# Kernel optimization log

Hardware: AMD Instinct MI355X
Metric: run time of the kernel (lower is better)

## Reference

```python
import jax, jax.numpy as jnp
import numpy as np

N_NODES = 50000
N_EDGES = 800000
F_IN = 128
HIDDEN = 256
N_CLASSES = 4


def setup_inputs() -> dict:
    key = jax.random.key(0)
    k1, k2, k3, k4 = jax.random.split(key, 4)
    x = jax.random.normal(k1, (N_NODES, F_IN), dtype=jnp.float32)
    edge_index = jax.random.randint(k2, (2, N_EDGES), 0, N_NODES, dtype=jnp.int64)
    # Glorot-style init for the two GCNConv linear layers (PyG GCNConv: W then bias)
    s1 = (6.0 / (F_IN + HIDDEN)) ** 0.5
    s2 = (6.0 / (HIDDEN + N_CLASSES)) ** 0.5
    W1 = jax.random.uniform(k3, (F_IN, HIDDEN), jnp.float32, -s1, s1)
    W2 = jax.random.uniform(k4, (HIDDEN, N_CLASSES), jnp.float32, -s2, s2)
    b1 = jnp.zeros((HIDDEN,), jnp.float32)
    b2 = jnp.zeros((N_CLASSES,), jnp.float32)
    return {"x": x, "edge_index": edge_index, "W1": W1, "b1": b1, "W2": W2, "b2": b2}


def _gcn_conv(x, W, b, src, dst, n_nodes):
    # PyG GCNConv: h = x @ W; add self-loops; symmetric D^{-1/2}(A+I)D^{-1/2} aggregation; + bias
    h = x @ W                                            # [N, out]
    deg = jnp.zeros((n_nodes,), h.dtype).at[dst].add(1.0) + 1.0  # +1 for self-loop
    dis = jax.lax.rsqrt(deg)                             # deg^{-1/2}
    norm = dis[src] * dis[dst]                           # [E]
    msg = norm[:, None] * h[src]                         # [E, out] per-edge messages
    agg = jax.ops.segment_sum(msg, dst, num_segments=n_nodes)
    agg = agg + (dis * dis)[:, None] * h                 # self-loop contribution
    return agg + b


def reference(x, edge_index, W1, b1, W2, b2):
    src, dst = edge_index[0], edge_index[1]
    h = _gcn_conv(x, W1, b1, src, dst, N_NODES)
    h = jax.nn.relu(h)
    # F.dropout with training=False (eval/inference reference) is identity
    out = _gcn_conv(h, W2, b2, src, dst, N_NODES)
    return out
```

## Files before the change

### kernel.cpp

```cpp
#include <hip/hip_runtime.h>

#define F_IN   128
#define HIDDEN 256
#define NCLS   4

#define BSH    7
#define BNODES 128
#define BCAP   3072
#define CHUNK  4096

typedef __attribute__((ext_vector_type(8))) short short8;
typedef __attribute__((ext_vector_type(4))) float f32x4;

__device__ __forceinline__ unsigned short f2bf(float f) {
    unsigned int u = __float_as_uint(f);
    return (unsigned short)((u + 0x7fffu + ((u >> 16) & 1u)) >> 16);
}

__device__ __forceinline__ float bflo(unsigned int u) { return __uint_as_float(u << 16); }
__device__ __forceinline__ float bfhi(unsigned int u) { return __uint_as_float(u & 0xffff0000u); }


__global__ __launch_bounds__(256) void k_bin(const int* __restrict__ srcIdx,
                                             const int* __restrict__ dstIdx,
                                             int* __restrict__ cursor,
                                             unsigned int* __restrict__ inter,
                                             int E, int nbuk) {
    __shared__ int cntS[512], bA[512], bB[512], curS[512], eS[512], gS[512];
    __shared__ unsigned int stag[CHUNK];
    __shared__ unsigned short bb[CHUNK];
    int t = threadIdx.x;
    int e0 = blockIdx.x * CHUNK;
    int n = E - e0; if (n > CHUNK) n = CHUNK;

    cntS[t] = 0; cntS[t + 256] = 0;
    __syncthreads();
    for (int i = t; i < n; i += 256)
        atomicAdd(&cntS[dstIdx[e0 + i] >> BSH], 1);
    __syncthreads();

    int* pa = bA; int* pb = bB;
    bA[t] = cntS[t]; bA[t + 256] = cntS[t + 256];
    __syncthreads();
    for (int off = 1; off < 512; off <<= 1) {
        pb[t] = pa[t] + (t >= off ? pa[t - off] : 0);
        int p1 = t + 256;
        pb[p1] = pa[p1] + (p1 >= off ? pa[p1 - off] : 0);
        __syncthreads();
        int* tmp = pa; pa = pb; pb = tmp;
    }
    eS[t] = pa[t] - cntS[t];
    curS[t] = eS[t];
    int p1 = t + 256;
    eS[p1] = pa[p1] - cntS[p1];
    curS[p1] = eS[p1];
    __syncthreads();

    for (int i = t; i < nbuk; i += 256) {
        int c = cntS[i];
        gS[i] = (c > 0) ? atomicAdd(&cursor[i], c) : 0;
    }
    __syncthreads();

    for (int i = t; i < n; i += 256) {
        int d = dstIdx[e0 + i];
        int s = srcIdx[e0 + i];
        int b = d >> BSH;
        unsigned int w = ((unsigned int)(d & (BNODES - 1)) << 16) | (unsigned int)s;
        int off = atomicAdd(&curS[b], 1);
        stag[off] = w;
        bb[off] = (unsigned short)b;
    }
    __syncthreads();

    for (int i = t; i < n; i += 256) {
        int b = bb[i];
        inter[(size_t)b * BCAP + gS[b] + (i - eS[b])] = stag[i];
    }
}


__global__ __launch_bounds__(512) void k_scan_buckets(const int* __restrict__ cursor,
                                                      int* __restrict__ base, int nbuk) {
    __shared__ int A[512], B[512];
    int t = threadIdx.x;
    int v = (t < nbuk) ? cursor[t] : 0;
    int* pa = A; int* pb = B;
    A[t] = v;
    __syncthreads();
    for (int off = 1; off < 512; off <<= 1) {
        pb[t] = pa[t] + (t >= off ? pa[t - off] : 0);
        __syncthreads();
        int* tmp = pa; pa = pb; pb = tmp;
    }
    if (t < nbuk) base[t] = pa[t] - v;
}


__global__ __launch_bounds__(256) void k_bucket_build(const unsigned int* __restrict__ inter,
                                                      const int* __restrict__ cursor,
                                                      const int* __restrict__ base,
                                                      const float2* __restrict__ x2,
                                                      int* __restrict__ rowptr,
                                                      float* __restrict__ dis,
                                                      unsigned int* __restrict__ xs,
                                                      unsigned short* __restrict__ csr16,
                                                      int N, int E, int nbuk) {
    __shared__ int cntS[BNODES], A[BNODES], B[BNODES], curS[BNODES];
    __shared__ float disS[BNODES];
    int t = threadIdx.x;
    int b = blockIdx.x;
    int node0 = b << BSH;
    int nloc = N - node0; if (nloc > BNODES) nloc = BNODES;
    int cntb = cursor[b];
    int gB = base[b];
    const unsigned int* ip = inter + (size_t)b * BCAP;

    if (t < BNODES) cntS[t] = 0;
    __syncthreads();
    for (int i = t; i < cntb; i += 256)
        atomicAdd(&cntS[ip[i] >> 16], 1);
    __syncthreads();

    int* pa = A; int* pb = B;
    if (t < BNODES) A[t] = cntS[t];
    __syncthreads();
    for (int off = 1; off < BNODES; off <<= 1) {
        if (t < BNODES) pb[t] = pa[t] + (t >= off ? pa[t - off] : 0);
        __syncthreads();
        int* tmp = pa; pa = pb; pb = tmp;
    }
    if (t < BNODES) {
        int excl = pa[t] - cntS[t];
        curS[t] = excl;
        int node = node0 + t;
        if (node < N) {
            rowptr[node] = gB + excl;
            float d = rsqrtf((float)cntS[t] + 1.0f);
            dis[node] = d;
            disS[t] = d;
        }
    }
    if (b == 0 && t == 0) rowptr[N] = E;
    __syncthreads();

    for (int i = t; i < cntb; i += 256) {
        unsigned int w = ip[i];
        int off = atomicAdd(&curS[w >> 16], 1);
        csr16[gB + off] = (unsigned short)(w & 0xffffu);
    }

    for (int i = t; i < nloc * 64; i += 256) {
        int nl = i >> 6, l = i & 63;
        float d = disS[nl];
        float2 v = x2[((size_t)(node0 + nl)) * 64 + l];
        xs[((size_t)(node0 + nl)) * 64 + l] =
            (unsigned int)f2bf(d * v.x) | ((unsigned int)f2bf(d * v.y) << 16);
    }
}


__global__ __launch_bounds__(256) void k_w1f(const float* __restrict__ W1,
                                             unsigned short* __restrict__ W1f) {
    int t = blockIdx.x * 256 + threadIdx.x;
    int lane = t & 63;
    int ks = (t >> 6) & 3;
    int ct = t >> 8;
    int n = ct * 16 + (lane & 15);
    int k0 = ks * 32 + (lane >> 4) * 8;
    unsigned int w[4];
#pragma unroll
    for (int p = 0; p < 4; ++p) {
        unsigned int lo = f2bf(W1[(k0 + 2 * p + 0) * HIDDEN + n]);
        unsigned int hi = f2bf(W1[(k0 + 2 * p + 1) * HIDDEN + n]);
        w[p] = lo | (hi << 16);
    }
    *(uint4*)(W1f + (size_t)t * 8) = make_uint4(w[0], w[1], w[2], w[3]);
}


__global__ __launch_bounds__(256) void k_pull_x(const int* __restrict__ rowptr,
                                                const unsigned short* __restrict__ csr16,
                                                const float* __restrict__ dis,
                                                const unsigned int* __restrict__ xs,
                                                const float2* __restrict__ x2,
                                                unsigned int* __restrict__ aggB, int N) {
    int wave = threadIdx.x >> 6;
    int node = blockIdx.x * 4 + wave;
    int l = threadIdx.x & 63;
    if (node >= N) return;
    int beg = rowptr[node];
    int end = rowptr[node + 1];
    float ax = 0.f, ay = 0.f;
    int e = beg;
    for (; e + 7 < end; e += 8) {
        int s0 = csr16[e + 0], s1 = csr16[e + 1], s2 = csr16[e + 2], s3 = csr16[e + 3];
        int s4 = csr16[e + 4], s5 = csr16[e + 5], s6 = csr16[e + 6], s7 = csr16[e + 7];
        unsigned int u0 = xs[(size_t)s0 * 64 + l];
        unsigned int u1 = xs[(size_t)s1 * 64 + l];
        unsigned int u2 = xs[(size_t)s2 * 64 + l];
        unsigned int u3 = xs[(size_t)s3 * 64 + l];
        unsigned int u4 = xs[(size_t)s4 * 64 + l];
        unsigned int u5 = xs[(size_t)s5 * 64 + l];
        unsigned int u6 = xs[(size_t)s6 * 64 + l];
        unsigned int u7 = xs[(size_t)s7 * 64 + l];
        ax += bflo(u0) + bflo(u1) + bflo(u2) + bflo(u3) + bflo(u4) + bflo(u5) + bflo(u6) + bflo(u7);
        ay += bfhi(u0) + bfhi(u1) + bfhi(u2) + bfhi(u3) + bfhi(u4) + bfhi(u5) + bfhi(u6) + bfhi(u7);
    }
    for (; e < end; ++e) {
        unsigned int u = xs[(size_t)csr16[e] * 64 + l];
        ax += bflo(u);
        ay += bfhi(u);
    }
    float dd = dis[node];
    float sd = dd * dd;
    float2 xv = x2[(size_t)node * 64 + l];
    float ox = dd * ax + sd * xv.x;
    float oy = dd * ay + sd * xv.y;
    aggB[(size_t)node * 64 + l] = (unsigned int)f2bf(ox) | ((unsigned int)f2bf(oy) << 16);
}


__global__ __launch_bounds__(256) void k_gemm_mfma(const unsigned short* __restrict__ aggB,
                                                   const unsigned short* __restrict__ W1f,
                                                   const float* __restrict__ b1,
                                                   const float* __restrict__ W2,
                                                   float* __restrict__ Z, int N) {
    int wave = threadIdx.x >> 6;
    int lane = threadIdx.x & 63;
    int tile = blockIdx.x * 4 + wave;
    int row0 = tile * 16;
    if (row0 >= N) return;
    int q = lane >> 4;
    int c16 = lane & 15;

    short8 a[4];
    const unsigned short* arow = aggB + (size_t)(row0 + c16) * F_IN;
#pragma unroll
    for (int ks = 0; ks < 4; ++ks)
        a[ks] = *(const short8*)(arow + ks * 32 + q * 8);

    float p[4][4] = {{0.f}};
#pragma unroll
    for (int ct = 0; ct < 16; ++ct) {
        f32x4 c = {0.f, 0.f, 0.f, 0.f};
#pragma unroll
        for (int ks = 0; ks < 4; ++ks) {
            short8 b = *(const short8*)(W1f + ((size_t)((ct * 4 + ks) * 64 + lane)) * 8);
            c = __builtin_amdgcn_mfma_f32_16x16x32_bf16(a[ks], b, c, 0, 0, 0);
        }
        int n = ct * 16 + c16;
        float bias = b1[n];
        float4 w2v = *(const float4*)(W2 + n * NCLS);
#pragma unroll
        for (int r = 0; r < 4; ++r) {
            float h = c[r] + bias;
            h = h > 0.f ? h : 0.f;
            p[r][0] += h * w2v.x;
            p[r][1] += h * w2v.y;
            p[r][2] += h * w2v.z;
            p[r][3] += h * w2v.w;
        }
    }
#pragma unroll
    for (int m = 1; m < 16; m <<= 1) {
#pragma unroll
        for (int r = 0; r < 4; ++r) {
#pragma unroll
            for (int j = 0; j < 4; ++j)
                p[r][j] += __shfl_xor(p[r][j], m);
        }
    }
    if (c16 == 0) {
#pragma unroll
        for (int r = 0; r < 4; ++r) {
            int row = row0 + q * 4 + r;
            *(float4*)(Z + (size_t)row * NCLS) = make_float4(p[r][0], p[r][1], p[r][2], p[r][3]);
        }
    }
}


__global__ __launch_bounds__(256) void k_pull_z(const int* __restrict__ rowptr,
                                                const unsigned short* __restrict__ csr16,
                                                const float* __restrict__ dis,
                                                const float* __restrict__ Z,
                                                const float* __restrict__ b2,
                                                float* __restrict__ out, int N) {
    int t = blockIdx.x * blockDim.x + threadIdx.x;
    int node = t >> 2;
    int j = t & 3;
    if (node >= N) return;
    int beg = rowptr[node];
    int end = rowptr[node + 1];
    float acc = 0.f;
    for (int e = beg; e < end; ++e) {
        int s = csr16[e];
        acc += dis[s] * Z[(size_t)s * NCLS + j];
    }
    float dd = dis[node];
    out[(size_t)node * NCLS + j] = dd * acc + dd * dd * Z[(size_t)node * NCLS + j] + b2[j];
}


extern "C" void kernel_launch(void* const* d_in, const int* in_sizes, int n_in,
                              void* d_out, int out_size, void* d_ws, size_t ws_size,
                              hipStream_t stream) {
    const float* x      = (const float*)d_in[0];
    const int*   ei     = (const int*)d_in[1];
    const float* W1     = (const float*)d_in[2];
    const float* b1     = (const float*)d_in[3];
    const float* W2     = (const float*)d_in[4];
    const float* b2     = (const float*)d_in[5];
    float* out          = (float*)d_out;

    const int N = in_sizes[0] / F_IN;
    const int E = in_sizes[1] / 2;
    const int* srcIdx = ei;
    const int* dstIdx = ei + E;

    const int nbuk = (N + BNODES - 1) >> BSH;

    unsigned short* aggB = (unsigned short*)d_ws;
    unsigned short* xsB  = aggB + (size_t)N * F_IN;
    unsigned short* W1f  = xsB + (size_t)N * F_IN;
    float* Z    = (float*)(W1f + 32768);
    float* dis  = Z + (size_t)N * NCLS;
    int* rowptr = (int*)(dis + N);
    int* cursor = rowptr + N + 1;
    int* bucketBase = cursor + nbuk;
    unsigned short* csr16 = (unsigned short*)(bucketBase + nbuk);
    unsigned int* inter = (unsigned int*)(csr16 + ((E + 1) & ~1));

    hipMemsetAsync(cursor, 0, (size_t)nbuk * sizeof(int), stream);
    k_bin<<<(E + CHUNK - 1) / CHUNK, 256, 0, stream>>>(srcIdx, dstIdx, cursor, inter, E, nbuk);
    k_scan_buckets<<<1, 512, 0, stream>>>(cursor, bucketBase, nbuk);
    k_bucket_build<<<nbuk, 256, 0, stream>>>(inter, cursor, bucketBase, (const float2*)x,
                                             rowptr, dis, (unsigned int*)xsB, csr16, N, E, nbuk);

    k_w1f<<<16, 256, 0, stream>>>(W1, W1f);
    k_pull_x<<<(N + 3) / 4, 256, 0, stream>>>(rowptr, csr16, dis, (const unsigned int*)xsB,
                                              (const float2*)x, (unsigned int*)aggB, N);

    const int nTiles = (N + 15) / 16;
    k_gemm_mfma<<<(nTiles + 3) / 4, 256, 0, stream>>>(aggB, W1f, b1, W2, Z, N);

    k_pull_z<<<(N * 4 + 255) / 256, 256, 0, stream>>>(rowptr, csr16, dis, Z, b2, out, N);
}
```

Measured before the change: 183.3 us.

## Fuse neighbor aggregation with MFMA GEMM and fold scan and memset into kernels

Merges the layer-1 gather aggregation and the bf16 MFMA GEMM into one kernel that stages 32 aggregated rows in LDS, then splits the 16 hidden column tiles across 4 waves and reduces the partial layer-2 projections through shared memory. This removes the aggB round trip through global memory and one launch. The bucket prefix scan is recomputed inside each bucket_build block by summing the preceding cursors, and the cursor memset is folded into the W1 conversion kernel, which drops two more launches. The cost is less parallelism per block during the gather phase, since each wave now handles 8 nodes in sequence, and redundant per-block scan reads.

```diff
diff --git a/kernel.cpp b/kernel.cpp
--- a/kernel.cpp
+++ b/kernel.cpp
@@ -8,6 +8,7 @@
 #define BNODES 128
 #define BCAP   3072
 #define CHUNK  4096
+#define MROWS  32
 
 typedef __attribute__((ext_vector_type(8))) short short8;
 typedef __attribute__((ext_vector_type(4))) float f32x4;
@@ -80,41 +81,33 @@
 }
 
 
-__global__ __launch_bounds__(512) void k_scan_buckets(const int* __restrict__ cursor,
-                                                      int* __restrict__ base, int nbuk) {
-    __shared__ int A[512], B[512];
-    int t = threadIdx.x;
-    int v = (t < nbuk) ? cursor[t] : 0;
-    int* pa = A; int* pb = B;
-    A[t] = v;
-    __syncthreads();
-    for (int off = 1; off < 512; off <<= 1) {
-        pb[t] = pa[t] + (t >= off ? pa[t - off] : 0);
-        __syncthreads();
-        int* tmp = pa; pa = pb; pb = tmp;
-    }
-    if (t < nbuk) base[t] = pa[t] - v;
-}
-
-
 __global__ __launch_bounds__(256) void k_bucket_build(const unsigned int* __restrict__ inter,
                                                       const int* __restrict__ cursor,
-                                                      const int* __restrict__ base,
                                                       const float2* __restrict__ x2,
                                                       int* __restrict__ rowptr,
                                                       float* __restrict__ dis,
                                                       unsigned int* __restrict__ xs,
                                                       unsigned short* __restrict__ csr16,
                                                       int N, int E, int nbuk) {
-    __shared__ int cntS[BNODES], A[BNODES], B[BNODES], curS[BNODES];
+    __shared__ int cntS[BNODES], A[BNODES], B[BNODES], curS[BNODES], red[256];
     __shared__ float disS[BNODES];
     int t = threadIdx.x;
     int b = blockIdx.x;
     int node0 = b << BSH;
     int nloc = N - node0; if (nloc > BNODES) nloc = BNODES;
     int cntb = cursor[b];
-    int gB = base[b];
     const unsigned int* ip = inter + (size_t)b * BCAP;
+
+    int partial = 0;
+    for (int i = t; i < b; i += 256) partial += cursor[i];
+    red[t] = partial;
+    __syncthreads();
+    for (int off = 128; off > 0; off >>= 1) {
+        if (t < off) red[t] += red[t + off];
+        __syncthreads();
+    }
+    int gB = red[0];
+    __syncthreads();
 
     if (t < BNODES) cntS[t] = 0;
     __syncthreads();
@@ -160,9 +153,11 @@
 }
 
 
-__global__ __launch_bounds__(256) void k_w1f(const float* __restrict__ W1,
-                                             unsigned short* __restrict__ W1f) {
+__global__ __launch_bounds__(256) void k_w1f_zero(const float* __restrict__ W1,
+                                                  unsigned short* __restrict__ W1f,
+                                                  int* __restrict__ cursor, int nbuk) {
     int t = blockIdx.x * 256 + threadIdx.x;
+    if (t < nbuk) cursor[t] = 0;
     int lane = t & 63;
     int ks = (t >> 6) & 3;
     int ct = t >> 8;
@@ -179,87 +174,89 @@
 }
 
 
-__global__ __launch_bounds__(256) void k_pull_x(const int* __restrict__ rowptr,
-                                                const unsigned short* __restrict__ csr16,
-                                                const float* __restrict__ dis,
-                                                const unsigned int* __restrict__ xs,
-                                                const float2* __restrict__ x2,
-                                                unsigned int* __restrict__ aggB, int N) {
-    int wave = threadIdx.x >> 6;
-    int node = blockIdx.x * 4 + wave;
-    int l = threadIdx.x & 63;
-    if (node >= N) return;
-    int beg = rowptr[node];
-    int end = rowptr[node + 1];
-    float ax = 0.f, ay = 0.f;
-    int e = beg;
-    for (; e + 7 < end; e += 8) {
-        int s0 = csr16[e + 0], s1 = csr16[e + 1], s2 = csr16[e + 2], s3 = csr16[e + 3];
-        int s4 = csr16[e + 4], s5 = csr16[e + 5], s6 = csr16[e + 6], s7 = csr16[e + 7];
-        unsigned int u0 = xs[(size_t)s0 * 64 + l];
-        unsigned int u1 = xs[(size_t)s1 * 64 + l];
-        unsigned int u2 = xs[(size_t)s2 * 64 + l];
-        unsigned int u3 = xs[(size_t)s3 * 64 + l];
-        unsigned int u4 = xs[(size_t)s4 * 64 + l];
-        unsigned int u5 = xs[(size_t)s5 * 64 + l];
-        unsigned int u6 = xs[(size_t)s6 * 64 + l];
-        unsigned int u7 = xs[(size_t)s7 * 64 + l];
-        ax += bflo(u0) + bflo(u1) + bflo(u2) + bflo(u3) + bflo(u4) + bflo(u5) + bflo(u6) + bflo(u7);
-        ay += bfhi(u0) + bfhi(u1) + bfhi(u2) + bfhi(u3) + bfhi(u4) + bfhi(u5) + bfhi(u6) + bfhi(u7);
-    }
-    for (; e < end; ++e) {
-        unsigned int u = xs[(size_t)csr16[e] * 64 + l];
-        ax += bflo(u);
-        ay += bfhi(u);
-    }
-    float dd = dis[node];
-    float sd = dd * dd;
-    float2 xv = x2[(size_t)node * 64 + l];
-    float ox = dd * ax + sd * xv.x;
-    float oy = dd * ay + sd * xv.y;
-    aggB[(size_t)node * 64 + l] = (unsigned int)f2bf(ox) | ((unsigned int)f2bf(oy) << 16);
-}
-
-
-__global__ __launch_bounds__(256) void k_gemm_mfma(const unsigned short* __restrict__ aggB,
-                                                   const unsigned short* __restrict__ W1f,
-                                                   const float* __restrict__ b1,
-                                                   const float* __restrict__ W2,
-                                                   float* __restrict__ Z, int N) {
-    int wave = threadIdx.x >> 6;
-    int lane = threadIdx.x & 63;
-    int tile = blockIdx.x * 4 + wave;
-    int row0 = tile * 16;
-    if (row0 >= N) return;
-    int q = lane >> 4;
-    int c16 = lane & 15;
-
-    short8 a[4];
-    const unsigned short* arow = aggB + (size_t)(row0 + c16) * F_IN;
-#pragma unroll
-    for (int ks = 0; ks < 4; ++ks)
-        a[ks] = *(const short8*)(arow + ks * 32 + q * 8);
-
-    float p[4][4] = {{0.f}};
-#pragma unroll
-    for (int ct = 0; ct < 16; ++ct) {
-        f32x4 c = {0.f, 0.f, 0.f, 0.f};
+__global__ __launch_bounds__(256) void k_fused(const int* __restrict__ rowptr,
+                                               const unsigned short* __restrict__ csr16,
+                                               const float* __restrict__ dis,
+                                               const unsigned int* __restrict__ xs,
+                                               const float2* __restrict__ x2,
+                                               const unsigned short* __restrict__ W1f,
+                                               const float* __restrict__ b1,
+                                               const float* __restrict__ W2,
+                                               float* __restrict__ Z, int N) {
+    __shared__ unsigned int As[MROWS][68];
+    __shared__ float zred[4][2][16][4];
+    int t = threadIdx.x;
+    int wave = t >> 6, lane = t & 63;
+    int node0 = blockIdx.x * MROWS;
+
+#pragma unroll
+    for (int i = 0; i < 8; ++i) {
+        int m = wave * 8 + i;
+        int node = node0 + m;
+        if (node < N) {
+            int beg = rowptr[node];
+            int end = rowptr[node + 1];
+            float ax = 0.f, ay = 0.f;
+            int e = beg;
+            for (; e + 7 < end; e += 8) {
+                int s0 = csr16[e + 0], s1 = csr16[e + 1], s2 = csr16[e + 2], s3 = csr16[e + 3];
+                int s4 = csr16[e + 4], s5 = csr16[e + 5], s6 = csr16[e + 6], s7 = csr16[e + 7];
+                unsigned int u0 = xs[(size_t)s0 * 64 + lane];
+                unsigned int u1 = xs[(size_t)s1 * 64 + lane];
+                unsigned int u2 = xs[(size_t)s2 * 64 + lane];
+                unsigned int u3 = xs[(size_t)s3 * 64 + lane];
+                unsigned int u4 = xs[(size_t)s4 * 64 + lane];
+                unsigned int u5 = xs[(size_t)s5 * 64 + lane];
+                unsigned int u6 = xs[(size_t)s6 * 64 + lane];
+                unsigned int u7 = xs[(size_t)s7 * 64 + lane];
+                ax += bflo(u0) + bflo(u1) + bflo(u2) + bflo(u3) + bflo(u4) + bflo(u5) + bflo(u6) + bflo(u7);
+                ay += bfhi(u0) + bfhi(u1) + bfhi(u2) + bfhi(u3) + bfhi(u4) + bfhi(u5) + bfhi(u6) + bfhi(u7);
+            }
+            for (; e < end; ++e) {
+                unsigned int u = xs[(size_t)csr16[e] * 64 + lane];
+                ax += bflo(u);
+                ay += bfhi(u);
+            }
+            float dd = dis[node];
+            float sd = dd * dd;
+            float2 xv = x2[(size_t)node * 64 + lane];
+            float ox = dd * ax + sd * xv.x;
+            float oy = dd * ay + sd * xv.y;
+            As[m][lane] = (unsigned int)f2bf(ox) | ((unsigned int)f2bf(oy) << 16);
+        } else {
+            As[m][lane] = 0;
+        }
+    }
+    __syncthreads();
+
+    int q = lane >> 4, c16 = lane & 15;
+    short8 a0[4], a1[4];
+#pragma unroll
+    for (int ks = 0; ks < 4; ++ks) {
+        a0[ks] = *(const short8*)&As[c16][ks * 16 + q * 4];
+        a1[ks] = *(const short8*)&As[c16 + 16][ks * 16 + q * 4];
+    }
+    float p0[4][4] = {{0.f}}, p1[4][4] = {{0.f}};
+#pragma unroll
+    for (int cc = 0; cc < 4; ++cc) {
+        int ct = wave * 4 + cc;
+        f32x4 c0 = {0.f, 0.f, 0.f, 0.f};
+        f32x4 c1 = {0.f, 0.f, 0.f, 0.f};
 #pragma unroll
         for (int ks = 0; ks < 4; ++ks) {
             short8 b = *(const short8*)(W1f + ((size_t)((ct * 4 + ks) * 64 + lane)) * 8);
-            c = __builtin_amdgcn_mfma_f32_16x16x32_bf16(a[ks], b, c, 0, 0, 0);
+            c0 = __builtin_amdgcn_mfma_f32_16x16x32_bf16(a0[ks], b, c0, 0, 0, 0);
+            c1 = __builtin_amdgcn_mfma_f32_16x16x32_bf16(a1[ks], b, c1, 0, 0, 0);
         }
         int n = ct * 16 + c16;
         float bias = b1[n];
         float4 w2v = *(const float4*)(W2 + n * NCLS);
 #pragma unroll
         for (int r = 0; r < 4; ++r) {
-            float h = c[r] + bias;
-            h = h > 0.f ? h : 0.f;
-            p[r][0] += h * w2v.x;
-            p[r][1] += h * w2v.y;
-            p[r][2] += h * w2v.z;
-            p[r][3] += h * w2v.w;
+            float h0 = c0[r] + bias; h0 = h0 > 0.f ? h0 : 0.f;
+            float h1 = c1[r] + bias; h1 = h1 > 0.f ? h1 : 0.f;
+            p0[r][0] += h0 * w2v.x; p0[r][1] += h0 * w2v.y; p0[r][2] += h0 * w2v.z; p0[r][3] += h0 * w2v.w;
+            p1[r][0] += h1 * w2v.x; p1[r][1] += h1 * w2v.y; p1[r][2] += h1 * w2v.z; p1[r][3] += h1 * w2v.w;
         }
     }
 #pragma unroll
@@ -267,16 +264,30 @@
 #pragma unroll
         for (int r = 0; r < 4; ++r) {
 #pragma unroll
-            for (int j = 0; j < 4; ++j)
-                p[r][j] += __shfl_xor(p[r][j], m);
+            for (int j = 0; j < 4; ++j) {
+                p0[r][j] += __shfl_xor(p0[r][j], m);
+                p1[r][j] += __shfl_xor(p1[r][j], m);
+            }
         }
     }
     if (c16 == 0) {
 #pragma unroll
         for (int r = 0; r < 4; ++r) {
-            int row = row0 + q * 4 + r;
-            *(float4*)(Z + (size_t)row * NCLS) = make_float4(p[r][0], p[r][1], p[r][2], p[r][3]);
-        }
+#pragma unroll
+            for (int j = 0; j < 4; ++j) {
+                zred[wave][0][q * 4 + r][j] = p0[r][j];
+                zred[wave][1][q * 4 + r][j] = p1[r][j];
+            }
+        }
+    }
+    __syncthreads();
+    if (t < 128) {
+        int row = t >> 2, j = t & 3;
+        int tile = row >> 4, r16 = row & 15;
+        float s = zred[0][tile][r16][j] + zred[1][tile][r16][j] +
+                  zred[2][tile][r16][j] + zred[3][tile][r16][j];
+        int grow = node0 + row;
+        if (grow < N) Z[(size_t)grow * NCLS + j] = s;
     }
 }
 
@@ -321,29 +332,21 @@
 
     const int nbuk = (N + BNODES - 1) >> BSH;
 
-    unsigned short* aggB = (unsigned short*)d_ws;
-    unsigned short* xsB  = aggB + (size_t)N * F_IN;
+    unsigned short* xsB  = (unsigned short*)d_ws;
     unsigned short* W1f  = xsB + (size_t)N * F_IN;
     float* Z    = (float*)(W1f + 32768);
     float* dis  = Z + (size_t)N * NCLS;
     int* rowptr = (int*)(dis + N);
     int* cursor = rowptr + N + 1;
-    int* bucketBase = cursor + nbuk;
-    unsigned short* csr16 = (unsigned short*)(bucketBase + nbuk);
+    unsigned short* csr16 = (unsigned short*)(cursor + nbuk);
     unsigned int* inter = (unsigned int*)(csr16 + ((E + 1) & ~1));
 
-    hipMemsetAsync(cursor, 0, (size_t)nbuk * sizeof(int), stream);
+    k_w1f_zero<<<16, 256, 0, stream>>>(W1, W1f, cursor, nbuk);
     k_bin<<<(E + CHUNK - 1) / CHUNK, 256, 0, stream>>>(srcIdx, dstIdx, cursor, inter, E, nbuk);
-    k_scan_buckets<<<1, 512, 0, stream>>>(cursor, bucketBase, nbuk);
-    k_bucket_build<<<nbuk, 256, 0, stream>>>(inter, cursor, bucketBase, (const float2*)x,
+    k_bucket_build<<<nbuk, 256, 0, stream>>>(inter, cursor, (const float2*)x,
                                              rowptr, dis, (unsigned int*)xsB, csr16, N, E, nbuk);
-
-    k_w1f<<<16, 256, 0, stream>>>(W1, W1f);
-    k_pull_x<<<(N + 3) / 4, 256, 0, stream>>>(rowptr, csr16, dis, (const unsigned int*)xsB,
-                                              (const float2*)x, (unsigned int*)aggB, N);
-
-    const int nTiles = (N + 15) / 16;
-    k_gemm_mfma<<<(nTiles + 3) / 4, 256, 0, stream>>>(aggB, W1f, b1, W2, Z, N);
-
+    k_fused<<<(N + MROWS - 1) / MROWS, 256, 0, stream>>>(rowptr, csr16, dis,
+                                                         (const unsigned int*)xsB, (const float2*)x,
+                                                         W1f, b1, W2, Z, N);
     k_pull_z<<<(N * 4 + 255) / 256, 256, 0, stream>>>(rowptr, csr16, dis, Z, b2, out, N);
 }
```

After: 200.5 us. 9.4% more time.

## Replace CSR with fixed-capacity padded per-node neighbor lists and sorted indices

Applied to the files above, without the earlier changes.

Drops the global bucket scan and rowptr in favour of a fixed 64-slot neighbor array per node, padded to a multiple of 8 with a dummy zero node N. Each list is sorted by insertion sort in shared memory for gather locality, and the pull kernels read neighbors with 16-byte vector loads and no remainder loop. The memset and the W1 conversion launch are merged into one kernel, removing launches. The cost is a hard cap of 64 in-degree per node, which could overflow for high-degree nodes, plus wasted gathers on the padding slots.

```diff
diff --git a/kernel.cpp b/kernel.cpp
--- a/kernel.cpp
+++ b/kernel.cpp
@@ -8,6 +8,7 @@
 #define BNODES 128
 #define BCAP   3072
 #define CHUNK  4096
+#define NCAP   64
 
 typedef __attribute__((ext_vector_type(8))) short short8;
 typedef __attribute__((ext_vector_type(4))) float f32x4;
@@ -80,74 +81,68 @@
 }
 
 
-__global__ __launch_bounds__(512) void k_scan_buckets(const int* __restrict__ cursor,
-                                                      int* __restrict__ base, int nbuk) {
-    __shared__ int A[512], B[512];
-    int t = threadIdx.x;
-    int v = (t < nbuk) ? cursor[t] : 0;
-    int* pa = A; int* pb = B;
-    A[t] = v;
-    __syncthreads();
-    for (int off = 1; off < 512; off <<= 1) {
-        pb[t] = pa[t] + (t >= off ? pa[t - off] : 0);
-        __syncthreads();
-        int* tmp = pa; pa = pb; pb = tmp;
-    }
-    if (t < nbuk) base[t] = pa[t] - v;
-}
-
-
 __global__ __launch_bounds__(256) void k_bucket_build(const unsigned int* __restrict__ inter,
                                                       const int* __restrict__ cursor,
-                                                      const int* __restrict__ base,
                                                       const float2* __restrict__ x2,
-                                                      int* __restrict__ rowptr,
                                                       float* __restrict__ dis,
+                                                      int* __restrict__ degPad,
                                                       unsigned int* __restrict__ xs,
                                                       unsigned short* __restrict__ csr16,
-                                                      int N, int E, int nbuk) {
-    __shared__ int cntS[BNODES], A[BNODES], B[BNODES], curS[BNODES];
+                                                      int N, int nbuk) {
+    __shared__ int cntS[BNODES], curS[BNODES];
     __shared__ float disS[BNODES];
+    __shared__ __align__(16) unsigned short csrS[BNODES * NCAP];
     int t = threadIdx.x;
     int b = blockIdx.x;
     int node0 = b << BSH;
     int nloc = N - node0; if (nloc > BNODES) nloc = BNODES;
     int cntb = cursor[b];
-    int gB = base[b];
     const unsigned int* ip = inter + (size_t)b * BCAP;
 
-    if (t < BNODES) cntS[t] = 0;
+    if (t < BNODES) { cntS[t] = 0; curS[t] = 0; }
     __syncthreads();
     for (int i = t; i < cntb; i += 256)
         atomicAdd(&cntS[ip[i] >> 16], 1);
     __syncthreads();
 
-    int* pa = A; int* pb = B;
-    if (t < BNODES) A[t] = cntS[t];
-    __syncthreads();
-    for (int off = 1; off < BNODES; off <<= 1) {
-        if (t < BNODES) pb[t] = pa[t] + (t >= off ? pa[t - off] : 0);
-        __syncthreads();
-        int* tmp = pa; pa = pb; pb = tmp;
-    }
-    if (t < BNODES) {
-        int excl = pa[t] - cntS[t];
-        curS[t] = excl;
-        int node = node0 + t;
-        if (node < N) {
-            rowptr[node] = gB + excl;
-            float d = rsqrtf((float)cntS[t] + 1.0f);
-            dis[node] = d;
-            disS[t] = d;
-        }
-    }
-    if (b == 0 && t == 0) rowptr[N] = E;
+    if (t < nloc) {
+        int c = cntS[t];
+        float d = rsqrtf((float)c + 1.0f);
+        dis[node0 + t] = d;
+        disS[t] = d;
+        degPad[node0 + t] = (c + 7) & ~7;
+    }
     __syncthreads();
 
     for (int i = t; i < cntb; i += 256) {
         unsigned int w = ip[i];
-        int off = atomicAdd(&curS[w >> 16], 1);
-        csr16[gB + off] = (unsigned short)(w & 0xffffu);
+        int nl = w >> 16;
+        int off = atomicAdd(&curS[nl], 1);
+        csrS[nl * NCAP + off] = (unsigned short)(w & 0xffffu);
+    }
+    __syncthreads();
+
+    if (t < nloc) {
+        unsigned short* a = &csrS[t * NCAP];
+        int c = cntS[t];
+        for (int i = 1; i < c; ++i) {
+            unsigned short key = a[i];
+            int j = i - 1;
+            while (j >= 0 && a[j] > key) { a[j + 1] = a[j]; --j; }
+            a[j + 1] = key;
+        }
+        int p = (c + 7) & ~7;
+        for (int k = c; k < p; ++k) a[k] = (unsigned short)N;
+    }
+    __syncthreads();
+
+    for (int g = t; g < nloc * (NCAP / 8); g += 256) {
+        int nl = g >> 3;
+        int sl = (g & 7) * 8;
+        if (sl < ((cntS[nl] + 7) & ~7)) {
+            *(uint4*)&csr16[((size_t)(node0 + nl)) * NCAP + sl] =
+                *(const uint4*)&csrS[nl * NCAP + sl];
+        }
     }
 
     for (int i = t; i < nloc * 64; i += 256) {
@@ -157,12 +152,18 @@
         xs[((size_t)(node0 + nl)) * 64 + l] =
             (unsigned int)f2bf(d * v.x) | ((unsigned int)f2bf(d * v.y) << 16);
     }
-}
-
-
-__global__ __launch_bounds__(256) void k_w1f(const float* __restrict__ W1,
-                                             unsigned short* __restrict__ W1f) {
+    if (b == 0) {
+        if (t < 64) xs[(size_t)N * 64 + t] = 0u;
+        if (t == 64) dis[N] = 0.f;
+    }
+}
+
+
+__global__ __launch_bounds__(256) void k_w1f_zero(const float* __restrict__ W1,
+                                                  unsigned short* __restrict__ W1f,
+                                                  int* __restrict__ cursor, int nbuk) {
     int t = blockIdx.x * 256 + threadIdx.x;
+    if (t < nbuk) cursor[t] = 0;
     int lane = t & 63;
     int ks = (t >> 6) & 3;
     int ct = t >> 8;
@@ -179,8 +180,8 @@
 }
 
 
-__global__ __launch_bounds__(256) void k_pull_x(const int* __restrict__ rowptr,
-                                                const unsigned short* __restrict__ csr16,
+__global__ __launch_bounds__(256) void k_pull_x(const unsigned short* __restrict__ csr16,
+                                                const int* __restrict__ degPad,
                                                 const float* __restrict__ dis,
                                                 const unsigned int* __restrict__ xs,
                                                 const float2* __restrict__ x2,
@@ -189,13 +190,15 @@
     int node = blockIdx.x * 4 + wave;
     int l = threadIdx.x & 63;
     if (node >= N) return;
-    int beg = rowptr[node];
-    int end = rowptr[node + 1];
+    int dp = degPad[node];
+    const unsigned short* cp = csr16 + (size_t)node * NCAP;
     float ax = 0.f, ay = 0.f;
-    int e = beg;
-    for (; e + 7 < end; e += 8) {
-        int s0 = csr16[e + 0], s1 = csr16[e + 1], s2 = csr16[e + 2], s3 = csr16[e + 3];
-        int s4 = csr16[e + 4], s5 = csr16[e + 5], s6 = csr16[e + 6], s7 = csr16[e + 7];
+    for (int e = 0; e < dp; e += 8) {
+        uint4 iv = *(const uint4*)(cp + e);
+        int s0 = iv.x & 0xffff, s1 = iv.x >> 16;
+        int s2 = iv.y & 0xffff, s3 = iv.y >> 16;
+        int s4 = iv.z & 0xffff, s5 = iv.z >> 16;
+        int s6 = iv.w & 0xffff, s7 = iv.w >> 16;
         unsigned int u0 = xs[(size_t)s0 * 64 + l];
         unsigned int u1 = xs[(size_t)s1 * 64 + l];
         unsigned int u2 = xs[(size_t)s2 * 64 + l];
@@ -207,11 +210,6 @@
         ax += bflo(u0) + bflo(u1) + bflo(u2) + bflo(u3) + bflo(u4) + bflo(u5) + bflo(u6) + bflo(u7);
         ay += bfhi(u0) + bfhi(u1) + bfhi(u2) + bfhi(u3) + bfhi(u4) + bfhi(u5) + bfhi(u6) + bfhi(u7);
     }
-    for (; e < end; ++e) {
-        unsigned int u = xs[(size_t)csr16[e] * 64 + l];
-        ax += bflo(u);
-        ay += bfhi(u);
-    }
     float dd = dis[node];
     float sd = dd * dd;
     float2 xv = x2[(size_t)node * 64 + l];
@@ -230,7 +228,7 @@
     int lane = threadIdx.x & 63;
     int tile = blockIdx.x * 4 + wave;
     int row0 = tile * 16;
-    if (row0 >= N) return;
+    if (row0 > N) return;
     int q = lane >> 4;
     int c16 = lane & 15;
 
@@ -275,14 +273,17 @@
 #pragma unroll
         for (int r = 0; r < 4; ++r) {
             int row = row0 + q * 4 + r;
-            *(float4*)(Z + (size_t)row * NCLS) = make_float4(p[r][0], p[r][1], p[r][2], p[r][3]);
-        }
-    }
-}
-
-
-__global__ __launch_bounds__(256) void k_pull_z(const int* __restrict__ rowptr,
-                                                const unsigned short* __restrict__ csr16,
+            if (row < N)
+                *(float4*)(Z + (size_t)row * NCLS) = make_float4(p[r][0], p[r][1], p[r][2], p[r][3]);
+            else if (row == N)
+                *(float4*)(Z + (size_t)row * NCLS) = make_float4(0.f, 0.f, 0.f, 0.f);
+        }
+    }
+}
+
+
+__global__ __launch_bounds__(256) void k_pull_z(const unsigned short* __restrict__ csr16,
+                                                const int* __restrict__ degPad,
                                                 const float* __restrict__ dis,
                                                 const float* __restrict__ Z,
                                                 const float* __restrict__ b2,
@@ -291,12 +292,19 @@
     int node = t >> 2;
     int j = t & 3;
     if (node >= N) return;
-    int beg = rowptr[node];
-    int end = rowptr[node + 1];
+    int dp = degPad[node];
+    const unsigned short* cp = csr16 + (size_t)node * NCAP;
     float acc = 0.f;
-    for (int e = beg; e < end; ++e) {
-        int s = csr16[e];
-        acc += dis[s] * Z[(size_t)s * NCLS + j];
+    for (int e = 0; e < dp; e += 8) {
+        uint4 iv = *(const uint4*)(cp + e);
+        int s0 = iv.x & 0xffff, s1 = iv.x >> 16;
+        int s2 = iv.y & 0xffff, s3 = iv.y >> 16;
+        int s4 = iv.z & 0xffff, s5 = iv.z >> 16;
+        int s6 = iv.w & 0xffff, s7 = iv.w >> 16;
+        acc += dis[s0] * Z[(size_t)s0 * NCLS + j] + dis[s1] * Z[(size_t)s1 * NCLS + j]
+             + dis[s2] * Z[(size_t)s2 * NCLS + j] + dis[s3] * Z[(size_t)s3 * NCLS + j]
+             + dis[s4] * Z[(size_t)s4 * NCLS + j] + dis[s5] * Z[(size_t)s5 * NCLS + j]
+             + dis[s6] * Z[(size_t)s6 * NCLS + j] + dis[s7] * Z[(size_t)s7 * NCLS + j];
     }
     float dd = dis[node];
     out[(size_t)node * NCLS + j] = dd * acc + dd * dd * Z[(size_t)node * NCLS + j] + b2[j];
@@ -322,28 +330,22 @@
     const int nbuk = (N + BNODES - 1) >> BSH;
 
     unsigned short* aggB = (unsigned short*)d_ws;
-    unsigned short* xsB  = aggB + (size_t)N * F_IN;
-    unsigned short* W1f  = xsB + (size_t)N * F_IN;
+    unsigned short* xsB  = aggB + (size_t)(N + 16) * F_IN;
+    unsigned short* W1f  = xsB + (size_t)(N + 8) * F_IN;
     float* Z    = (float*)(W1f + 32768);
-    float* dis  = Z + (size_t)N * NCLS;
-    int* rowptr = (int*)(dis + N);
-    int* cursor = rowptr + N + 1;
-    int* bucketBase = cursor + nbuk;
-    unsigned short* csr16 = (unsigned short*)(bucketBase + nbuk);
-    unsigned int* inter = (unsigned int*)(csr16 + ((E + 1) & ~1));
-
-    hipMemsetAsync(cursor, 0, (size_t)nbuk * sizeof(int), stream);
+    float* dis  = Z + (size_t)(N + 4) * NCLS;
+    int* degPad = (int*)(dis + N + 4);
+    int* cursor = degPad + N;
+    unsigned short* csr16 = (unsigned short*)(cursor + 512);
+    unsigned int* inter = (unsigned int*)(csr16 + (size_t)N * NCAP);
+
+    k_w1f_zero<<<16, 256, 0, stream>>>(W1, W1f, cursor, nbuk);
     k_bin<<<(E + CHUNK - 1) / CHUNK, 256, 0, stream>>>(srcIdx, dstIdx, cursor, inter, E, nbuk);
-    k_scan_buckets<<<1, 512, 0, stream>>>(cursor, bucketBase, nbuk);
-    k_bucket_build<<<nbuk, 256, 0, stream>>>(inter, cursor, bucketBase, (const float2*)x,
-                                             rowptr, dis, (unsigned int*)xsB, csr16, N, E, nbuk);
-
-    k_w1f<<<16, 256, 0, stream>>>(W1, W1f);
-    k_pull_x<<<(N + 3) / 4, 256, 0, stream>>>(rowptr, csr16, dis, (const unsigned int*)xsB,
+    k_bucket_build<<<nbuk, 256, 0, stream>>>(inter, cursor, (const float2*)x,
+                                             dis, degPad, (unsigned int*)xsB, csr16, N, nbuk);
+    k_pull_x<<<(N + 3) / 4, 256, 0, stream>>>(csr16, degPad, dis, (const unsigned int*)xsB,
                                               (const float2*)x, (unsigned int*)aggB, N);
-
-    const int nTiles = (N + 15) / 16;
+    const int nTiles = N / 16 + 1;
     k_gemm_mfma<<<(nTiles + 3) / 4, 256, 0, stream>>>(aggB, W1f, b1, W2, Z, N);
-
-    k_pull_z<<<(N * 4 + 255) / 256, 256, 0, stream>>>(rowptr, csr16, dis, Z, b2, out, N);
-}
+    k_pull_z<<<(N * 4 + 255) / 256, 256, 0, stream>>>(csr16, degPad, dis, Z, b2, out, N);
+}
```

New measurement: 206.6 us. +12.7%, slower.
